# Kernel optimization log

Measured on AMD Instinct MI355X. Metric: run time of the kernel, lower is better.

Reference implementation:

```python
import jax, jax.numpy as jnp
import numpy as np

D_MODEL = 1024
STATE = 64
HEADS = 8
EXPAND = 2
INNER = EXPAND * D_MODEL          # 2048
HEAD_DIM = INNER // HEADS         # 256
PROJ_OUT = 2 * INNER + 2 * STATE + HEADS  # z, x, B, C, dt
BATCH, SEQ = 2, 1024
EPS = 1e-5


def setup_inputs() -> dict:
    key = jax.random.key(0)
    ks = jax.random.split(key, 6)
    g = lambda k, shape, sc: jax.random.normal(k, shape, jnp.float32) * sc
    return {
        "input_tensor": jax.random.normal(ks[0], (BATCH, SEQ, D_MODEL), jnp.float32),
        "ln_gamma": jnp.ones((D_MODEL,), jnp.float32),
        "ln_beta": jnp.zeros((D_MODEL,), jnp.float32),
        "W_in": g(ks[1], (D_MODEL, PROJ_OUT), 0.02),
        "b_in": jnp.zeros((PROJ_OUT,), jnp.float32),
        "A_log": jnp.log(jnp.arange(1, HEADS + 1, dtype=jnp.float32)),
        "D_skip": jnp.ones((HEADS,), jnp.float32),
        "dt_bias": g(ks[2], (HEADS,), 0.1),
        "W_out": g(ks[3], (INNER, D_MODEL), 0.02),
        "b_out": jnp.zeros((D_MODEL,), jnp.float32),
    }


def _layer_norm(x, gamma, beta):
    mu = jnp.mean(x, axis=-1, keepdims=True)
    xc = x - mu
    var = jnp.mean(xc * xc, axis=-1, keepdims=True)
    return xc * jax.lax.rsqrt(var + EPS) * gamma + beta


def _mamba2(u, W_in, b_in, A_log, D_skip, dt_bias, W_out, b_out):
    B, L, _ = u.shape
    zxbcdt = u @ W_in + b_in                                    # [B,L,PROJ_OUT]
    z = zxbcdt[..., :INNER]                                     # gate [B,L,INNER]
    xs = zxbcdt[..., INNER:2 * INNER].reshape(B, L, HEADS, HEAD_DIM)
    Bm = zxbcdt[..., 2 * INNER:2 * INNER + STATE]               # [B,L,N]
    Cm = zxbcdt[..., 2 * INNER + STATE:2 * INNER + 2 * STATE]   # [B,L,N]
    dt = jax.nn.softplus(zxbcdt[..., 2 * INNER + 2 * STATE:] + dt_bias)  # [B,L,H]

    A = -jnp.exp(A_log)                                         # [H], negative
    decay = jnp.exp(dt * A)                                     # [B,L,H]
    dtx = dt[..., None] * xs                                    # [B,L,H,P]

    # selective scan over time; state h: [B,H,P,N]
    def step(h, inp):
        dec_t, dtx_t, B_t, C_t = inp                            # [B,H],[B,H,P],[B,N],[B,N]
        h = dec_t[:, :, None, None] * h + dtx_t[..., None] * B_t[:, None, None, :]
        y = jnp.einsum('bhpn,bn->bhp', h, C_t)
        return h, y

    h0 = jnp.zeros((B, HEADS, HEAD_DIM, STATE), u.dtype)
    scan_in = (
        jnp.moveaxis(decay, 1, 0),   # [L,B,H]
        jnp.moveaxis(dtx, 1, 0),     # [L,B,H,P]
        jnp.moveaxis(Bm, 1, 0),      # [L,B,N]
        jnp.moveaxis(Cm, 1, 0),      # [L,B,N]
    )
    _, ys = jax.lax.scan(step, h0, scan_in)                     # [L,B,H,P]
    y = jnp.moveaxis(ys, 0, 1)                                  # [B,L,H,P]
    y = y + D_skip[None, None, :, None] * xs                    # skip connection
    y = y.reshape(B, L, INNER) * jax.nn.silu(z)                 # gated
    return y @ W_out + b_out


def reference(input_tensor, ln_gamma, ln_beta, W_in, b_in, A_log, D_skip, dt_bias, W_out, b_out):
    normed = _layer_norm(input_tensor, ln_gamma, ln_beta)
    out = _mamba2(normed, W_in, b_in, A_log, D_skip, dt_bias, W_out, b_out)
    return input_tensor + out
```

## Files before the change

### kernel.cpp

```cpp
#include <hip/hip_runtime.h>
#include <math.h>

#define D_MODEL 1024
#define STATE 64
#define HEADS 8
#define INNER 2048
#define HEAD_DIM 256
#define PROJ_OUT 4232
#define DT_OFF  4224
#define NPAD 4352
#define BATCH 2
#define SEQ 1024
#define NROWS (BATCH*SEQ)
#define EPS 1e-5f
#define BH (BATCH * HEADS)
#define LQ 32
#define NCH (SEQ / LQ)

typedef short s16x8 __attribute__((ext_vector_type(8)));
typedef float f32x4 __attribute__((ext_vector_type(4)));

#define LDS_AS(p) ((__attribute__((address_space(3))) void*)(p))
#define GLB_AS(p) ((const __attribute__((address_space(1))) void*)(p))

__device__ inline unsigned short f2bf(float f) {
    unsigned int u = __float_as_uint(f);
    unsigned int r = (u + 0x7fffu + ((u >> 16) & 1u)) >> 16;
    return (unsigned short)r;
}
__device__ inline float bf2f(unsigned short s) {
    return __uint_as_float(((unsigned int)s) << 16);
}
__device__ inline f32x4 mfma16(s16x8 a, s16x8 b, f32x4 c) {
    return __builtin_amdgcn_mfma_f32_16x16x32_bf16(a, b, c, 0, 0, 0);
}

__global__ __launch_bounds__(256) void ln_kernel(
    const float* __restrict__ x, const float* __restrict__ gamma,
    const float* __restrict__ beta, unsigned short* __restrict__ out)
{
    int row = blockIdx.x;
    int tid = threadIdx.x;
    const float4* xr = (const float4*)(x + (size_t)row * D_MODEL);
    float4 v = xr[tid];
    float s  = v.x + v.y + v.z + v.w;
    float sq = v.x*v.x + v.y*v.y + v.z*v.z + v.w*v.w;
    #pragma unroll
    for (int off = 32; off > 0; off >>= 1) {
        s  += __shfl_down(s,  off, 64);
        sq += __shfl_down(sq, off, 64);
    }
    __shared__ float ls[4], lq[4];
    int wave = tid >> 6, lane = tid & 63;
    if (lane == 0) { ls[wave] = s; lq[wave] = sq; }
    __syncthreads();
    s  = ls[0] + ls[1] + ls[2] + ls[3];
    sq = lq[0] + lq[1] + lq[2] + lq[3];
    float mu  = s * (1.f / D_MODEL);
    float var = sq * (1.f / D_MODEL) - mu * mu;
    float rs  = rsqrtf(var + EPS);
    float4 g  = ((const float4*)gamma)[tid];
    float4 bb = ((const float4*)beta)[tid];
    ushort4 o;
    o.x = f2bf((v.x - mu) * rs * g.x + bb.x);
    o.y = f2bf((v.y - mu) * rs * g.y + bb.y);
    o.z = f2bf((v.z - mu) * rs * g.z + bb.z);
    o.w = f2bf((v.w - mu) * rs * g.w + bb.w);
    ((ushort4*)(out + (size_t)row * D_MODEL))[tid] = o;
}

__global__ __launch_bounds__(256) void transpose_bf16(
    const float* __restrict__ in, unsigned short* __restrict__ out,
    int R, int C)
{
    __shared__ float tile[32][33];
    int c0 = blockIdx.x * 32;
    int r0 = blockIdx.y * 32;
    int tx = threadIdx.x & 31;
    int ty = threadIdx.x >> 5;
    #pragma unroll
    for (int i = 0; i < 4; ++i) {
        int r = ty + i * 8;
        int gc = c0 + tx;
        tile[r][tx] = (gc < C) ? in[(size_t)(r0 + r) * C + gc] : 0.f;
    }
    __syncthreads();
    #pragma unroll
    for (int i = 0; i < 4; ++i) {
        int oc = ty + i * 8;
        out[(size_t)(c0 + oc) * R + r0 + tx] = f2bf(tile[tx][oc]);
    }
}

template<int BM, int BN, bool HAS_ADD, bool GUARD_N, bool OUT_BF16>
__global__ __launch_bounds__(256) void gemm_bf16(
    const unsigned short* __restrict__ A, const unsigned short* __restrict__ BT,
    const float* __restrict__ bias, const float* __restrict__ add,
    float* __restrict__ C, unsigned short* __restrict__ Cb,
    float* __restrict__ dtb, int Nreal, int Nstride, int K)
{
    constexpr int FM = BM / 32;
    constexpr int FN = BN / 32;
    constexpr int NL = BM / 64 + BN / 64;
    __shared__ unsigned short Asm[2][BM * 32];
    __shared__ unsigned short Bsm[2][BN * 32];
    const int tid = threadIdx.x;
    const int l = tid & 63, w = tid >> 6;
    const int lr = l & 15, lk = l >> 4;
    const int m0 = blockIdx.y * BM, n0 = blockIdx.x * BN;
    const int wm = w >> 1, wn = w & 1;

    f32x4 acc[FM][FN] = {};

    const unsigned short* Abase = A  + (size_t)(m0 + lr) * K + lk * 8;
    const unsigned short* Bbase = BT + (size_t)(n0 + lr) * K + lk * 8;

    auto stage = [&](int buf, int k0) {
        #pragma unroll
        for (int i = 0; i < BM / 64; ++i) {
            int mb = w + 4 * i;
            __builtin_amdgcn_global_load_lds(
                GLB_AS(Abase + (size_t)mb * 16 * K + k0),
                LDS_AS(&Asm[buf][mb * 512]), 16, 0, 0);
        }
        #pragma unroll
        for (int i = 0; i < BN / 64; ++i) {
            int nb = w + 4 * i;
            __builtin_amdgcn_global_load_lds(
                GLB_AS(Bbase + (size_t)nb * 16 * K + k0),
                LDS_AS(&Bsm[buf][nb * 512]), 16, 0, 0);
        }
    };

    stage(0, 0);
    int cur = 0;
    for (int k0 = 0; k0 < K; k0 += 32) {
        if (k0 + 32 < K) {
            stage(cur ^ 1, k0 + 32);
            if constexpr (NL == 4)
                asm volatile("s_waitcnt vmcnt(4)" ::: "memory");
            else
                asm volatile("s_waitcnt vmcnt(2)" ::: "memory");
        } else {
            asm volatile("s_waitcnt vmcnt(0)" ::: "memory");
        }
        __builtin_amdgcn_s_barrier();
        __builtin_amdgcn_sched_barrier(0);
        s16x8 af[FM], bfv[FN];
        #pragma unroll
        for (int i = 0; i < FM; ++i)
            af[i] = *(const s16x8*)&Asm[cur][((wm * FM + i) * 64 + l) * 8];
        #pragma unroll
        for (int j = 0; j < FN; ++j)
            bfv[j] = *(const s16x8*)&Bsm[cur][((wn * FN + j) * 64 + l) * 8];
        #pragma unroll
        for (int i = 0; i < FM; ++i)
            #pragma unroll
            for (int j = 0; j < FN; ++j)
                acc[i][j] = mfma16(af[i], bfv[j], acc[i][j]);
        __builtin_amdgcn_s_barrier();
        cur ^= 1;
    }

    #pragma unroll
    for (int i = 0; i < FM; ++i) {
        int row = m0 + (wm * FM + i) * 16 + lk * 4;
        #pragma unroll
        for (int j = 0; j < FN; ++j) {
            int col = n0 + (wn * FN + j) * 16 + lr;
            if (GUARD_N && col >= Nreal) continue;
            float bv = bias[col];
            #pragma unroll
            for (int r = 0; r < 4; ++r) {
                float v = acc[i][j][r] + bv;
                if (HAS_ADD) v += add[(size_t)(row + r) * Nstride + col];
                if (OUT_BF16) {
                    Cb[(size_t)(row + r) * Nstride + col] = f2bf(v);
                    if (col >= DT_OFF)
                        dtb[(size_t)(row + r) * HEADS + (col - DT_OFF)] = v;
                } else {
                    C[(size_t)(row + r) * Nstride + col] = v;
                }
            }
        }
    }
}

__global__ __launch_bounds__(256) void ssd_pass1(
    const unsigned short* __restrict__ zx, const float* __restrict__ dtbuf,
    const float* __restrict__ A_log, const float* __restrict__ dt_bias,
    unsigned short* __restrict__ Sbuf, float* __restrict__ Dk)
{
    __shared__ float w1s[LQ];
    __shared__ unsigned short xT[HEAD_DIM * LQ];
    __shared__ unsigned short BpT[STATE * LQ];
    int blk = blockIdx.x;
    int bh = blk >> 5, ck = blk & (NCH - 1);
    int b = bh >> 3, h = bh & 7;
    int tid = threadIdx.x;
    int l = tid & 63, w = tid >> 6;
    int lr = l & 15, lk = l >> 4;
    float a = -expf(A_log[h]);
    int t0 = ck * LQ;
    const unsigned short* zrow = zx + (size_t)(b * SEQ + t0) * PROJ_OUT;

    if (w == 0) {
        int tl = l & 31;
        float dtr = dtbuf[(size_t)(b * SEQ + t0 + tl) * HEADS + h] + dt_bias[h];
        float dtv = (dtr > 20.f) ? dtr : log1pf(expf(dtr));
        float c = dtv;
        #pragma unroll
        for (int off = 1; off < 32; off <<= 1) {
            float v = __shfl_up(c, off, 64);
            if ((l & 31) >= off) c += v;
        }
        float c31 = __shfl(c, 31, 64);
        if (l < 32) {
            w1s[l] = dtv * expf(a * (c31 - c));
            if (l == 31) Dk[bh * NCH + ck] = expf(a * c31);
        }
    }
    {
        int p = tid;
        const unsigned short* xp = zrow + INNER + h * HEAD_DIM + p;
        int sw = (p & 3) << 3;
        #pragma unroll
        for (int tp = 0; tp < 16; ++tp) {
            unsigned int x0 = xp[(size_t)(2 * tp) * PROJ_OUT];
            unsigned int x1 = xp[(size_t)(2 * tp + 1) * PROJ_OUT];
            *(unsigned int*)&xT[p * LQ + ((2 * tp) ^ sw)] = x0 | (x1 << 16);
        }
    }
    __syncthreads();
    #pragma unroll
    for (int i = 0; i < 8; ++i) {
        int e = i * 256 + tid;
        int t = e >> 6, n = e & 63;
        float v = bf2f(zrow[(size_t)t * PROJ_OUT + 2 * INNER + n]) * w1s[t];
        BpT[n * LQ + (t ^ ((n & 3) << 3))] = f2bf(v);
    }
    __syncthreads();

    f32x4 acc[4][4] = {};
    {
        int krun = lk * 8;
        s16x8 bfr[4];
        #pragma unroll
        for (int j = 0; j < 4; ++j) {
            int n = j * 16 + lr;
            bfr[j] = *(const s16x8*)&BpT[n * LQ + (krun ^ ((n & 3) << 3))];
        }
        #pragma unroll
        for (int i = 0; i < 4; ++i) {
            int p = (w * 4 + i) * 16 + lr;
            s16x8 afr = *(const s16x8*)&xT[p * LQ + (krun ^ ((p & 3) << 3))];
            #pragma unroll
            for (int j = 0; j < 4; ++j)
                acc[i][j] = mfma16(afr, bfr[j], acc[i][j]);
        }
    }
    unsigned short* sp = Sbuf + ((size_t)bh * NCH + ck) * (STATE * HEAD_DIM);
    #pragma unroll
    for (int i = 0; i < 4; ++i) {
        int p = (w * 4 + i) * 16 + lk * 4;
        #pragma unroll
        for (int j = 0; j < 4; ++j) {
            int n = j * 16 + lr;
            #pragma unroll
            for (int r = 0; r < 4; ++r)
                sp[(size_t)(p + r) * STATE + n] = f2bf(acc[i][j][r]);
        }
    }
}

template<int NCHq>
__global__ __launch_bounds__(256) void scan_combine(
    unsigned short* __restrict__ Sbuf, const float* __restrict__ Dk)
{
    int bh = blockIdx.y;
    int e  = blockIdx.x * 256 + threadIdx.x;
    size_t base = (size_t)bh * NCHq * (STATE * HEAD_DIM) + e;
    float h = 0.f;
    #pragma unroll 8
    for (int k = 0; k < NCHq; ++k) {
        size_t idx = base + (size_t)k * (STATE * HEAD_DIM);
        float s = bf2f(Sbuf[idx]);
        Sbuf[idx] = f2bf(h);
        h = Dk[bh * NCHq + k] * h + s;
    }
}

__global__ __launch_bounds__(256) void ssd_pass2(
    const unsigned short* __restrict__ zx, const float* __restrict__ dtbuf,
    const float* __restrict__ A_log, const float* __restrict__ D_skip,
    const float* __restrict__ dt_bias,
    const unsigned short* __restrict__ Sbuf, unsigned short* __restrict__ yg)
{
    __shared__ float dts[LQ], cums[LQ];
    __shared__ unsigned short xT[HEAD_DIM * LQ];
    __shared__ unsigned short Cm[LQ * STATE];
    __shared__ unsigned short Cd[LQ * STATE];
    __shared__ unsigned short Bm[LQ * STATE];
    __shared__ unsigned short Pp[LQ * LQ];
    int blk = blockIdx.x;
    int bh = blk >> 5, ck = blk & (NCH - 1);
    int b = bh >> 3, h = bh & 7;
    int tid = threadIdx.x;
    int l = tid & 63, w = tid >> 6;
    int lr = l & 15, lk = l >> 4;
    float a = -expf(A_log[h]);
    float dsk = D_skip[h];
    int t0 = ck * LQ;
    const unsigned short* zrow = zx + (size_t)(b * SEQ + t0) * PROJ_OUT;

    if (w == 0) {
        int tl = l & 31;
        float dtr = dtbuf[(size_t)(b * SEQ + t0 + tl) * HEADS + h] + dt_bias[h];
        float dtv = (dtr > 20.f) ? dtr : log1pf(expf(dtr));
        float c = dtv;
        #pragma unroll
        for (int off = 1; off < 32; off <<= 1) {
            float v = __shfl_up(c, off, 64);
            if ((l & 31) >= off) c += v;
        }
        if (l < 32) { dts[l] = dtv; cums[l] = c; }
    }
    {
        int p = tid;
        const unsigned short* xp = zrow + INNER + h * HEAD_DIM + p;
        int sw = (p & 3) << 3;
        #pragma unroll
        for (int tp = 0; tp < 16; ++tp) {
            unsigned int x0 = xp[(size_t)(2 * tp) * PROJ_OUT];
            unsigned int x1 = xp[(size_t)(2 * tp + 1) * PROJ_OUT];
            *(unsigned int*)&xT[p * LQ + ((2 * tp) ^ sw)] = x0 | (x1 << 16);
        }
    }
    __syncthreads();
    #pragma unroll
    for (int i = 0; i < 8; ++i) {
        int e = i * 256 + tid;
        int t = e >> 6, n = e & 63;
        int sn = n ^ ((t & 7) << 3);
        unsigned short cv = zrow[(size_t)t * PROJ_OUT + 2 * INNER + STATE + n];
        Cm[t * STATE + sn] = cv;
        Cd[t * STATE + sn] = f2bf(bf2f(cv) * expf(a * cums[t]));
        Bm[t * STATE + sn] = zrow[(size_t)t * PROJ_OUT + 2 * INNER + n];
    }
    __syncthreads();

    const unsigned short* hbase = Sbuf + ((size_t)bh * NCH + ck) * (STATE * HEAD_DIM);
    s16x8 h0f[4][2];
    #pragma unroll
    for (int j = 0; j < 4; ++j) {
        int p = w * 64 + j * 16 + lr;
        #pragma unroll
        for (int kk = 0; kk < 2; ++kk)
            h0f[j][kk] = *(const s16x8*)&hbase[(size_t)p * STATE + kk * 32 + lk * 8];
    }

    f32x4 pa = {};
    #pragma unroll
    for (int kk = 0; kk < 2; ++kk) {
        int krun = kk * 32 + lk * 8;
        int tA = (w >> 1) * 16 + lr;
        int sB = (w & 1) * 16 + lr;
        s16x8 afr = *(const s16x8*)&Cm[tA * STATE + (krun ^ ((tA & 7) << 3))];
        s16x8 bfr = *(const s16x8*)&Bm[sB * STATE + (krun ^ ((sB & 7) << 3))];
        pa = mfma16(afr, bfr, pa);
    }
    #pragma unroll
    for (int r = 0; r < 4; ++r) {
        int t = (w >> 1) * 16 + lk * 4 + r;
        int s = (w & 1) * 16 + lr;
        float sc = (s <= t) ? dts[s] * expf(a * (cums[t] - cums[s])) : 0.f;
        Pp[t * LQ + (s ^ ((t & 3) << 3))] = f2bf(pa[r] * sc);
    }
    __syncthreads();

    f32x4 ya[2][4] = {};
    {
        int krun = lk * 8;
        s16x8 bfr[4];
        #pragma unroll
        for (int j = 0; j < 4; ++j) {
            int p = w * 64 + j * 16 + lr;
            bfr[j] = *(const s16x8*)&xT[p * LQ + (krun ^ ((p & 3) << 3))];
        }
        #pragma unroll
        for (int i = 0; i < 2; ++i) {
            int t = i * 16 + lr;
            s16x8 afr = *(const s16x8*)&Pp[t * LQ + (krun ^ ((t & 3) << 3))];
            #pragma unroll
            for (int j = 0; j < 4; ++j)
                ya[i][j] = mfma16(afr, bfr[j], ya[i][j]);
        }
    }
    #pragma unroll
    for (int kk = 0; kk < 2; ++kk) {
        int krun = kk * 32 + lk * 8;
        #pragma unroll
        for (int i = 0; i < 2; ++i) {
            int t = i * 16 + lr;
            s16x8 afr = *(const s16x8*)&Cd[t * STATE + (krun ^ ((t & 7) << 3))];
            #pragma unroll
            for (int j = 0; j < 4; ++j)
                ya[i][j] = mfma16(afr, h0f[j][kk], ya[i][j]);
        }
    }

    #pragma unroll
    for (int i = 0; i < 2; ++i) {
        #pragma unroll
        for (int r = 0; r < 4; ++r) {
            int t = i * 16 + lk * 4 + r;
            #pragma unroll
            for (int j = 0; j < 4; ++j) {
                int p = w * 64 + j * 16 + lr;
                float xv = bf2f(xT[p * LQ + (t ^ ((p & 3) << 3))]);
                float z  = bf2f(zrow[(size_t)t * PROJ_OUT + h * HEAD_DIM + p]);
                float y = ya[i][j][r] + dsk * xv;
                float gate = z / (1.f + expf(-z));
                yg[(size_t)(b * SEQ + t0 + t) * INNER + h * HEAD_DIM + p] = f2bf(y * gate);
            }
        }
    }
}

__global__ __launch_bounds__(256) void scan_serial(
    const unsigned short* __restrict__ zx, const float* __restrict__ dtbuf,
    const float* __restrict__ A_log, const float* __restrict__ D_skip,
    const float* __restrict__ dt_bias,
    unsigned short* __restrict__ yg)
{
    int bh = blockIdx.x;
    int b  = bh >> 3, h = bh & 7;
    int p  = threadIdx.x;
    float a   = -expf(A_log[h]);
    float dsk = D_skip[h];
    float dtb = dt_bias[h];

    float hs[STATE];
    #pragma unroll
    for (int n = 0; n < STATE; ++n) hs[n] = 0.f;

    for (int t = 0; t < SEQ; ++t) {
        const unsigned short* row = zx + (size_t)(b * SEQ + t) * PROJ_OUT;
        float dtr = dtbuf[(size_t)(b * SEQ + t) * HEADS + h] + dtb;
        float dt  = (dtr > 20.f) ? dtr : log1pf(expf(dtr));
        float dec = expf(dt * a);
        float x   = bf2f(row[INNER + h * HEAD_DIM + p]);
        float z   = bf2f(row[h * HEAD_DIM + p]);
        float dtx = dt * x;
        #pragma unroll
        for (int n = 0; n < STATE; ++n)
            hs[n] = dec * hs[n] + dtx * bf2f(row[2 * INNER + n]);
        float y0 = 0.f;
        #pragma unroll
        for (int n = 0; n < STATE; ++n)
            y0 += hs[n] * bf2f(row[2 * INNER + STATE + n]);
        float y = y0 + dsk * x;
        float gate = z / (1.f + expf(-z));
        yg[(size_t)(b * SEQ + t) * INNER + h * HEAD_DIM + p] = f2bf(y * gate);
    }
}

extern "C" void kernel_launch(void* const* d_in, const int* in_sizes, int n_in,
                              void* d_out, int out_size, void* d_ws, size_t ws_size,
                              hipStream_t stream) {
    const float* input  = (const float*)d_in[0];
    const float* gamma  = (const float*)d_in[1];
    const float* beta   = (const float*)d_in[2];
    const float* W_in   = (const float*)d_in[3];
    const float* b_in   = (const float*)d_in[4];
    const float* A_log  = (const float*)d_in[5];
    const float* D_skip = (const float*)d_in[6];
    const float* dt_b   = (const float*)d_in[7];
    const float* W_out  = (const float*)d_in[8];
    const float* b_out  = (const float*)d_in[9];
    float* out = (float*)d_out;

    char* ws = (char*)d_ws;
    size_t off = 0;
    unsigned short* normed_bf = (unsigned short*)(ws + off); off += (size_t)NROWS * D_MODEL * 2;
    unsigned short* zx        = (unsigned short*)(ws + off); off += (size_t)NROWS * PROJ_OUT * 2;
    float*          dtbuf     = (float*)(ws + off);          off += (size_t)NROWS * HEADS * 4;
    unsigned short* yg        = (unsigned short*)(ws + off); off += (size_t)NROWS * INNER * 2;
    unsigned short* WT        = (unsigned short*)(ws + off); off += (size_t)NPAD * D_MODEL * 2;
    unsigned short* WoT       = (unsigned short*)(ws + off); off += (size_t)D_MODEL * INNER * 2;
    unsigned short* Sbuf      = (unsigned short*)(ws + off); off += (size_t)BH * NCH * STATE * HEAD_DIM * 2;
    off = (off + 255) & ~(size_t)255;
    float*          Dk        = (float*)(ws + off);          off += (size_t)BH * NCH * 4;
    bool ssd = (off <= ws_size);

    dim3 gt1(NPAD / 32, D_MODEL / 32);
    transpose_bf16<<<gt1, 256, 0, stream>>>(W_in, WT, D_MODEL, PROJ_OUT);
    dim3 gt2(D_MODEL / 32, INNER / 32);
    transpose_bf16<<<gt2, 256, 0, stream>>>(W_out, WoT, INNER, D_MODEL);

    ln_kernel<<<NROWS, 256, 0, stream>>>(input, gamma, beta, normed_bf);

    dim3 g1(NPAD / 128, NROWS / 128);
    gemm_bf16<128, 128, false, true, true><<<g1, 256, 0, stream>>>(
        normed_bf, WT, b_in, nullptr, nullptr, zx, dtbuf, PROJ_OUT, PROJ_OUT, D_MODEL);

    if (ssd) {
        ssd_pass1<<<BH * NCH, 256, 0, stream>>>(zx, dtbuf, A_log, dt_b, Sbuf, Dk);
        dim3 gc(STATE * HEAD_DIM / 256, BH);
        scan_combine<NCH><<<gc, 256, 0, stream>>>(Sbuf, Dk);
        ssd_pass2<<<BH * NCH, 256, 0, stream>>>(zx, dtbuf, A_log, D_skip, dt_b, Sbuf, yg);
    } else {
        scan_serial<<<BH, 256, 0, stream>>>(zx, dtbuf, A_log, D_skip, dt_b, yg);
    }

    dim3 g2(D_MODEL / 64, NROWS / 64);
    gemm_bf16<64, 64, true, false, false><<<g2, 256, 0, stream>>>(
        yg, WoT, b_out, input, out, nullptr, nullptr, D_MODEL, D_MODEL, INNER);
}
```

Before: 135.8 us.

## Add 256x256 eight-phase pipelined GEMM kernel for input projection

Replaces the 128x128 generic GEMM used for the input projection with a dedicated 512-thread kernel computing 256x256 output tiles. It uses K-tiles of 64, direct global-to-LDS loads, and four phases per K-step that interleave prefetching the next tile with MFMA work, raising MFMA priority via setprio. The goal is more data reuse per LDS load and better overlap of memory with compute. The cost is a much smaller grid (17x8 = 136 blocks), which may underfill the GPU's compute units, plus heavy register pressure and many barriers.

```diff
diff --git a/kernel.cpp b/kernel.cpp
--- a/kernel.cpp
+++ b/kernel.cpp
@@ -92,12 +92,110 @@
     }
 }
 
-template<int BM, int BN, bool HAS_ADD, bool GUARD_N, bool OUT_BF16>
+__global__ __launch_bounds__(512, 1) void gemm1_8ph(
+    const unsigned short* __restrict__ A, const unsigned short* __restrict__ BT,
+    const float* __restrict__ bias, unsigned short* __restrict__ Cb,
+    float* __restrict__ dtb)
+{
+    constexpr int K = D_MODEL;
+    constexpr int NT = K / 64;
+    __shared__ unsigned short Al[2][16384];
+    __shared__ unsigned short Bl[2][16384];
+    const int tid = threadIdx.x;
+    const int l = tid & 63, w = tid >> 6;
+    const int lr = l & 15, lk = l >> 4;
+    const int wm = w >> 2, wn = w & 3;
+    const int m0 = blockIdx.y * 256, n0 = blockIdx.x * 256;
+
+    f32x4 acc[8][4] = {};
+
+    const int sA = w * 4, k32s = sA & 1; (void)k32s;
+    auto stageA = [&](int buf, int kt, int p) {
+        int s = w * 4 + p, k32 = s & 1, mf = s >> 1;
+        __builtin_amdgcn_global_load_lds(
+            GLB_AS(A + (size_t)(m0 + mf * 16 + lr) * K + kt * 64 + k32 * 32 + lk * 8),
+            LDS_AS(&Al[buf][((k32 * 16 + mf) * 64 + l) * 8]), 16, 0, 0);
+    };
+    auto stageB = [&](int buf, int kt, int p) {
+        int s = w * 4 + p, k32 = s & 1, nf = s >> 1;
+        __builtin_amdgcn_global_load_lds(
+            GLB_AS(BT + (size_t)(n0 + nf * 16 + lr) * K + kt * 64 + k32 * 32 + lk * 8),
+            LDS_AS(&Bl[buf][((k32 * 16 + nf) * 64 + l) * 8]), 16, 0, 0);
+    };
+
+    #pragma unroll
+    for (int p = 0; p < 4; ++p) { stageA(0, 0, p); stageB(0, 0, p); }
+
+    for (int t = 0; t < NT; ++t) {
+        const int buf = t & 1, nbuf = buf ^ 1;
+        const bool pf = (t + 1 < NT);
+        asm volatile("s_waitcnt vmcnt(0)" ::: "memory");
+        __builtin_amdgcn_s_barrier();
+
+#define PHASE(MH, NH, P)                                                      \
+        {                                                                     \
+            s16x8 af[4][2], bfv[2][2];                                        \
+            _Pragma("unroll")                                                 \
+            for (int i = 0; i < 4; ++i) {                                     \
+                int mf = wm * 8 + (MH) * 4 + i;                               \
+                af[i][0] = *(const s16x8*)&Al[buf][((mf) * 64 + l) * 8];      \
+                af[i][1] = *(const s16x8*)&Al[buf][((16 + mf) * 64 + l) * 8]; \
+            }                                                                 \
+            _Pragma("unroll")                                                 \
+            for (int j = 0; j < 2; ++j) {                                     \
+                int nf = wn * 4 + (NH) * 2 + j;                               \
+                bfv[j][0] = *(const s16x8*)&Bl[buf][((nf) * 64 + l) * 8];     \
+                bfv[j][1] = *(const s16x8*)&Bl[buf][((16 + nf) * 64 + l) * 8];\
+            }                                                                 \
+            if (pf) { stageA(nbuf, t + 1, (P)); stageB(nbuf, t + 1, (P)); }   \
+            __builtin_amdgcn_s_barrier();                                     \
+            asm volatile("s_waitcnt lgkmcnt(0)" ::: "memory");                \
+            __builtin_amdgcn_sched_barrier(0);                                \
+            __builtin_amdgcn_s_setprio(1);                                    \
+            _Pragma("unroll")                                                 \
+            for (int i = 0; i < 4; ++i)                                       \
+                _Pragma("unroll")                                             \
+                for (int j = 0; j < 2; ++j) {                                 \
+                    acc[(MH)*4+i][(NH)*2+j] =                                 \
+                        mfma16(af[i][0], bfv[j][0], acc[(MH)*4+i][(NH)*2+j]); \
+                    acc[(MH)*4+i][(NH)*2+j] =                                 \
+                        mfma16(af[i][1], bfv[j][1], acc[(MH)*4+i][(NH)*2+j]); \
+                }                                                             \
+            __builtin_amdgcn_s_setprio(0);                                    \
+            __builtin_amdgcn_s_barrier();                                     \
+        }
+
+        PHASE(0, 0, 0)
+        PHASE(0, 1, 1)
+        PHASE(1, 0, 2)
+        PHASE(1, 1, 3)
+#undef PHASE
+    }
+
+    #pragma unroll
+    for (int mf = 0; mf < 8; ++mf) {
+        int row = m0 + (wm * 8 + mf) * 16 + lk * 4;
+        #pragma unroll
+        for (int nf = 0; nf < 4; ++nf) {
+            int col = n0 + (wn * 4 + nf) * 16 + lr;
+            if (col >= PROJ_OUT) continue;
+            float bv = bias[col];
+            #pragma unroll
+            for (int r = 0; r < 4; ++r) {
+                float v = acc[mf][nf][r] + bv;
+                Cb[(size_t)(row + r) * PROJ_OUT + col] = f2bf(v);
+                if (col >= DT_OFF)
+                    dtb[(size_t)(row + r) * HEADS + (col - DT_OFF)] = v;
+            }
+        }
+    }
+}
+
+template<int BM, int BN, bool HAS_ADD>
 __global__ __launch_bounds__(256) void gemm_bf16(
     const unsigned short* __restrict__ A, const unsigned short* __restrict__ BT,
     const float* __restrict__ bias, const float* __restrict__ add,
-    float* __restrict__ C, unsigned short* __restrict__ Cb,
-    float* __restrict__ dtb, int Nreal, int Nstride, int K)
+    float* __restrict__ C, int Nstride, int K)
 {
     constexpr int FM = BM / 32;
     constexpr int FN = BN / 32;
@@ -168,19 +266,12 @@
         #pragma unroll
         for (int j = 0; j < FN; ++j) {
             int col = n0 + (wn * FN + j) * 16 + lr;
-            if (GUARD_N && col >= Nreal) continue;
             float bv = bias[col];
             #pragma unroll
             for (int r = 0; r < 4; ++r) {
                 float v = acc[i][j][r] + bv;
                 if (HAS_ADD) v += add[(size_t)(row + r) * Nstride + col];
-                if (OUT_BF16) {
-                    Cb[(size_t)(row + r) * Nstride + col] = f2bf(v);
-                    if (col >= DT_OFF)
-                        dtb[(size_t)(row + r) * HEADS + (col - DT_OFF)] = v;
-                } else {
-                    C[(size_t)(row + r) * Nstride + col] = v;
-                }
+                C[(size_t)(row + r) * Nstride + col] = v;
             }
         }
     }
@@ -500,9 +591,8 @@
 
     ln_kernel<<<NROWS, 256, 0, stream>>>(input, gamma, beta, normed_bf);
 
-    dim3 g1(NPAD / 128, NROWS / 128);
-    gemm_bf16<128, 128, false, true, true><<<g1, 256, 0, stream>>>(
-        normed_bf, WT, b_in, nullptr, nullptr, zx, dtbuf, PROJ_OUT, PROJ_OUT, D_MODEL);
+    dim3 g1(NPAD / 256, NROWS / 256);
+    gemm1_8ph<<<g1, 512, 0, stream>>>(normed_bf, WT, b_in, zx, dtbuf);
 
     if (ssd) {
         ssd_pass1<<<BH * NCH, 256, 0, stream>>>(zx, dtbuf, A_log, dt_b, Sbuf, Dk);
@@ -514,6 +604,6 @@
     }
 
     dim3 g2(D_MODEL / 64, NROWS / 64);
-    gemm_bf16<64, 64, true, false, false><<<g2, 256, 0, stream>>>(
-        yg, WoT, b_out, input, out, nullptr, nullptr, D_MODEL, D_MODEL, INNER);
-}
+    gemm_bf16<64, 64, true><<<g2, 256, 0, stream>>>(
+        yg, WoT, b_out, input, out, D_MODEL, INNER);
+}
```

Result: no change. 135.8 us (-0.0%).
